# Performance work log

Hardware: AMD Instinct MI355X
Metric: run time of the kernel (lower is better)

The kernel has to match this reference:

```python
import jax, jax.numpy as jnp
import numpy as np

B, F, D_IN, D_K, D_V = 4, 4096, 1024, 128, 128


def setup_inputs() -> dict:
    key = jax.random.key(0)
    ks = jax.random.split(key, 7)
    s_in = 1.0 / np.sqrt(D_IN)
    x = jax.random.normal(ks[0], (B, F, D_IN), dtype=jnp.float32)
    # nn.Linear weights stored as (out, in); we keep (in, out) for x @ W
    Wq = jax.random.uniform(ks[1], (D_IN, D_K), jnp.float32, -s_in, s_in)
    bq = jax.random.uniform(ks[2], (D_K,), jnp.float32, -s_in, s_in)
    Wk = jax.random.uniform(ks[3], (D_IN, D_K), jnp.float32, -s_in, s_in)
    bk = jax.random.uniform(ks[4], (D_K,), jnp.float32, -s_in, s_in)
    Wv = jax.random.uniform(ks[5], (D_IN, D_V), jnp.float32, -s_in, s_in)
    bv = jax.random.uniform(ks[6], (D_V,), jnp.float32, -s_in, s_in)
    return {"x": x, "Wq": Wq, "bq": bq, "Wk": Wk, "bk": bk, "Wv": Wv, "bv": bv}


def reference(x, Wq, bq, Wk, bk, Wv, bv):
    Q = x @ Wq + bq  # (B, F, d_k)
    K = x @ Wk + bk  # (B, F, d_k)
    V = x @ Wv + bv  # (B, F, d_v)
    scale = 1.0 / jnp.sqrt(jnp.asarray(Q.shape[-1], Q.dtype))
    scores = jnp.einsum('bqd,bkd->bqk', Q, K) * scale  # (B, F, F)
    attn = jax.nn.softmax(scores, axis=-1)
    return jnp.einsum('bqk,bkd->bqd', attn, V)  # (B, F, d_v)
```

## Files before the change

### kernel.cpp

```cpp
#include <hip/hip_runtime.h>

#define TB 4
#define TF 4096
#define DIN 1024
#define DK 128
#define M_TOT (TB * TF)

typedef __attribute__((ext_vector_type(8))) short sh8;
typedef __attribute__((ext_vector_type(4))) float f32x4;

#if __has_builtin(__builtin_amdgcn_exp2f)
#define EXP2(x) __builtin_amdgcn_exp2f(x)
#else
#define EXP2(x) exp2f(x)
#endif

__device__ __forceinline__ unsigned short f2bf(float f) {
  unsigned int u = __builtin_bit_cast(unsigned int, f);
  u += 0x7FFFu + ((u >> 16) & 1u);
  return (unsigned short)(u >> 16);
}

__device__ __forceinline__ unsigned int pack_bf2(float a, float b) {
  return (unsigned int)f2bf(a) | ((unsigned int)f2bf(b) << 16);
}

__device__ __forceinline__ float bf2f(unsigned short u) {
  unsigned int x = ((unsigned int)u) << 16;
  return __builtin_bit_cast(float, x);
}

__global__ __launch_bounds__(256) void prep_wt_kernel(
    const float* __restrict__ Wq, const float* __restrict__ Wk,
    const float* __restrict__ Wv, unsigned short* __restrict__ Wf) {
  int idx = blockIdx.x * 256 + threadIdx.x;
  int j = idx & 7;
  int lane = (idx >> 3) & 63;
  int ks = (idx >> 9) & 31;
  int t = (idx >> 14) & 7;
  int p = idx >> 17;
  int col = t * 16 + (lane & 15);
  int k = ks * 32 + (lane >> 4) * 8 + j;
  const float* W = (p == 0) ? Wq : (p == 1) ? Wk : Wv;
  Wf[idx] = f2bf(W[k * DK + col]);
}

__global__ __launch_bounds__(512, 2) void proj_kernel(
    const float* __restrict__ x,
    const unsigned short* __restrict__ Wf,
    const float* __restrict__ bq, const float* __restrict__ bk,
    const float* __restrict__ bv,
    unsigned short* __restrict__ Qb,
    unsigned short* __restrict__ Kb,
    unsigned short* __restrict__ VT)
{
  const int tid = threadIdx.x;
  const int wave = tid >> 6;
  const int lane = tid & 63;
  const int lr = lane & 15;
  const int lg = lane >> 4;
  const int m0 = blockIdx.x * 64;
  const int col = wave * 16 + lr;

  __shared__ unsigned short Xlds[2][64 * 68];

  f32x4 acc[3][4];
  const f32x4 z4 = {0.f, 0.f, 0.f, 0.f};
#pragma unroll
  for (int p = 0; p < 3; ++p)
#pragma unroll
    for (int m = 0; m < 4; ++m) acc[p][m] = z4;

  const int xr = tid >> 3;
  const int xk8 = (tid & 7) * 8;
  const float* xrow = x + (size_t)(m0 + xr) * DIN + xk8;

  {
    const float4 f0 = *(const float4*)(xrow);
    const float4 f1 = *(const float4*)(xrow + 4);
    union { sh8 v; unsigned short u[8]; } U;
    U.u[0] = f2bf(f0.x); U.u[1] = f2bf(f0.y);
    U.u[2] = f2bf(f0.z); U.u[3] = f2bf(f0.w);
    U.u[4] = f2bf(f1.x); U.u[5] = f2bf(f1.y);
    U.u[6] = f2bf(f1.z); U.u[7] = f2bf(f1.w);
    *(sh8*)&Xlds[0][xr * 68 + xk8] = U.v;
  }
  __syncthreads();

  for (int t = 0; t < DIN / 64; ++t) {
    const int k0 = t * 64;
    const int cur = t & 1;

    if (t + 1 < DIN / 64) {
      const float4 f0 = *(const float4*)(xrow + k0 + 64);
      const float4 f1 = *(const float4*)(xrow + k0 + 68);
      union { sh8 v; unsigned short u[8]; } U;
      U.u[0] = f2bf(f0.x); U.u[1] = f2bf(f0.y);
      U.u[2] = f2bf(f0.z); U.u[3] = f2bf(f0.w);
      U.u[4] = f2bf(f1.x); U.u[5] = f2bf(f1.y);
      U.u[6] = f2bf(f1.z); U.u[7] = f2bf(f1.w);
      *(sh8*)&Xlds[cur ^ 1][xr * 68 + xk8] = U.v;
    }

    sh8 a[4][2];
#pragma unroll
    for (int m = 0; m < 4; ++m)
#pragma unroll
      for (int s = 0; s < 2; ++s)
        a[m][s] =
            *(const sh8*)&Xlds[cur][(m * 16 + lr) * 68 + s * 32 + lg * 8];
#pragma unroll
    for (int p = 0; p < 3; ++p) {
#pragma unroll
      for (int s = 0; s < 2; ++s) {
        sh8 b = *(const sh8*)(Wf +
                              ((size_t)((p * 8 + wave) * 32 + (k0 >> 5) + s)) *
                                  512 +
                              lane * 8);
#pragma unroll
        for (int m = 0; m < 4; ++m)
          acc[p][m] = __builtin_amdgcn_mfma_f32_16x16x32_bf16(a[m][s], b,
                                                              acc[p][m], 0, 0,
                                                              0);
      }
    }
    __syncthreads();
  }

  const float scale = 0.12751744f;
  const int b_idx = m0 >> 12;
  const float add_q = bq[col];
  const float add_k = bk[col];
  const float add_v = bv[col];
#pragma unroll
  for (int m = 0; m < 4; ++m) {
    const int rowbase = m0 + m * 16 + lg * 4;
#pragma unroll
    for (int r = 0; r < 4; ++r) {
      Qb[(size_t)(rowbase + r) * DK + col] =
          f2bf((acc[0][m][r] + add_q) * scale);
      Kb[(size_t)(rowbase + r) * DK + col] = f2bf(acc[1][m][r] + add_k);
    }
    const int fbase = (m0 & (TF - 1)) + m * 16 + lg * 4;
    ushort4 pv;
    pv.x = f2bf(acc[2][m][0] + add_v);
    pv.y = f2bf(acc[2][m][1] + add_v);
    pv.z = f2bf(acc[2][m][2] + add_v);
    pv.w = f2bf(acc[2][m][3] + add_v);
    *(ushort4*)(VT + ((size_t)b_idx * DK + col) * TF + fbase) = pv;
  }
}

template <int SPLIT>
__global__ __launch_bounds__(512, 2) void attn_part_kernel(
    const unsigned short* __restrict__ Qb, const unsigned short* __restrict__ Kb,
    const unsigned short* __restrict__ VT, unsigned short* __restrict__ Opart,
    float* __restrict__ Mpart, float* __restrict__ Lpart,
    float* __restrict__ out) {
  constexpr int CHUNK = TF / SPLIT;
  constexpr int NT = CHUNK / 64;
  const int tid = threadIdx.x;
  const int lane = tid & 63;
  const int lr = lane & 15;
  const int lg = lane >> 4;

  const int bid = blockIdx.x;
  const int xcd = bid & 7;
  const int batch = xcd >> 1;
  const int idb = ((bid >> 3) << 1) | (xcd & 1);
  const int slot = idb / SPLIT;
  const int chunk = idb % SPLIT;
  const int wave = tid >> 6;
  const int q0 = batch * TF + slot * 128 + wave * 16;
  const int kbase = chunk * CHUNK;

  __shared__ unsigned short Klds[2][64 * 136];
  __shared__ unsigned short Vlds[2][128 * 72];

  const unsigned short* Qp = Qb + (size_t)q0 * DK;
  const unsigned short* Kp = Kb + (size_t)batch * TF * DK;
  const unsigned short* Vp = VT + (size_t)batch * DK * TF;

  const int krow0 = tid >> 4, kc8 = tid & 15;
  const int vrow0 = tid >> 3, vc8 = tid & 7;

  sh8 aq[4];
#pragma unroll
  for (int dd = 0; dd < 4; ++dd)
    aq[dd] = *(const sh8*)(Qp + lr * DK + dd * 32 + lg * 8);

  const f32x4 z4 = {0.f, 0.f, 0.f, 0.f};
  f32x4 ot[8];
#pragma unroll
  for (int nb = 0; nb < 8; ++nb) ot[nb] = z4;
  float mrow = -1e30f, lrow = 0.f;

  const int srcA = lr + ((lane >> 4) & 1) * 32;
  const int srcB = srcA + 16;
  const bool chi = (lg >= 2);

#pragma unroll
  for (int i = 0; i < 2; ++i) {
    *(uint4*)&Klds[0][(krow0 + i * 32) * 136 + kc8 * 8] =
        *(const uint4*)(Kp + (size_t)(kbase + krow0 + i * 32) * DK + kc8 * 8);
    *(uint4*)&Vlds[0][(vrow0 + i * 64) * 72 + vc8 * 8] =
        *(const uint4*)(Vp + (size_t)(vrow0 + i * 64) * TF + kbase + vc8 * 8);
  }
  __syncthreads();

  for (int t = 0; t < NT; ++t) {
    const int kk0 = kbase + t * 64;
    const int cur = t & 1;

    if (t + 1 < NT) {
#pragma unroll
      for (int i = 0; i < 2; ++i) {
        *(uint4*)&Klds[cur ^ 1][(krow0 + i * 32) * 136 + kc8 * 8] =
            *(const uint4*)(Kp + (size_t)(kk0 + 64 + krow0 + i * 32) * DK +
                            kc8 * 8);
        *(uint4*)&Vlds[cur ^ 1][(vrow0 + i * 64) * 72 + vc8 * 8] =
            *(const uint4*)(Vp + (size_t)(vrow0 + i * 64) * TF + kk0 + 64 +
                            vc8 * 8);
      }
    }

    f32x4 st[4];
#pragma unroll
    for (int c = 0; c < 4; ++c) st[c] = z4;
    __builtin_amdgcn_s_setprio(1);
#pragma unroll
    for (int dd = 0; dd < 4; ++dd) {
#pragma unroll
      for (int c = 0; c < 4; ++c) {
        sh8 kb =
            *(const sh8*)&Klds[cur][(c * 16 + lr) * 136 + dd * 32 + lg * 8];
        st[c] =
            __builtin_amdgcn_mfma_f32_16x16x32_bf16(kb, aq[dd], st[c], 0, 0, 0);
      }
    }
    __builtin_amdgcn_s_setprio(0);

    float mx;
    {
      float m0a = fmaxf(fmaxf(st[0][0], st[0][1]), st[0][2]);
      float m0b = fmaxf(fmaxf(st[0][3], st[1][0]), st[1][1]);
      float m0c = fmaxf(fmaxf(st[1][2], st[1][3]), st[2][0]);
      float m0d = fmaxf(fmaxf(st[2][1], st[2][2]), st[2][3]);
      float m0e = fmaxf(fmaxf(st[3][0], st[3][1]), st[3][2]);
      float m1a = fmaxf(fmaxf(m0a, m0b), m0c);
      float m1b = fmaxf(fmaxf(m0d, m0e), st[3][3]);
      mx = fmaxf(m1a, m1b);
    }
    mx = fmaxf(mx, __shfl_xor(mx, 16));
    mx = fmaxf(mx, __shfl_xor(mx, 32));

    if (!__all(mx - mrow <= 11.5f)) {
      const float mnew = fmaxf(mrow, mx);
      const float al = EXP2(mrow - mnew);
      lrow *= al;
#pragma unroll
      for (int nb = 0; nb < 8; ++nb)
#pragma unroll
        for (int r = 0; r < 4; ++r) ot[nb][r] *= al;
      mrow = mnew;
    }

    float p[4][4];
    float rs = 0.f;
#pragma unroll
    for (int c = 0; c < 4; ++c)
#pragma unroll
      for (int r = 0; r < 4; ++r) {
        p[c][r] = EXP2(st[c][r] - mrow);
        rs += p[c][r];
      }
    rs += __shfl_xor(rs, 16);
    rs += __shfl_xor(rs, 32);
    lrow += rs;

    unsigned int up[4][2];
#pragma unroll
    for (int c = 0; c < 4; ++c) {
      up[c][0] = pack_bf2(p[c][0], p[c][1]);
      up[c][1] = pack_bf2(p[c][2], p[c][3]);
    }

#pragma unroll
    for (int ks = 0; ks < 2; ++ks) {
      unsigned int e0 = __shfl((int)up[2 * ks][0], srcA);
      unsigned int o0 = __shfl((int)up[2 * ks + 1][0], srcA);
      unsigned int e1 = __shfl((int)up[2 * ks][1], srcA);
      unsigned int o1 = __shfl((int)up[2 * ks + 1][1], srcA);
      unsigned int e2 = __shfl((int)up[2 * ks][0], srcB);
      unsigned int o2 = __shfl((int)up[2 * ks + 1][0], srcB);
      unsigned int e3 = __shfl((int)up[2 * ks][1], srcB);
      unsigned int o3 = __shfl((int)up[2 * ks + 1][1], srcB);
      union { unsigned int u[4]; sh8 v; } PA;
      PA.u[0] = chi ? o0 : e0;
      PA.u[1] = chi ? o1 : e1;
      PA.u[2] = chi ? o2 : e2;
      PA.u[3] = chi ? o3 : e3;
      __builtin_amdgcn_s_setprio(1);
#pragma unroll
      for (int nb = 0; nb < 8; ++nb) {
        sh8 vb =
            *(const sh8*)&Vlds[cur][(nb * 16 + lr) * 72 + ks * 32 + lg * 8];
        ot[nb] =
            __builtin_amdgcn_mfma_f32_16x16x32_bf16(vb, PA.v, ot[nb], 0, 0, 0);
      }
      __builtin_amdgcn_s_setprio(0);
    }

    __syncthreads();
  }

  if constexpr (SPLIT == 1) {
    const float inv = 1.0f / lrow;
#pragma unroll
    for (int nb = 0; nb < 8; ++nb) {
      float4 res = {ot[nb][0] * inv, ot[nb][1] * inv, ot[nb][2] * inv,
                    ot[nb][3] * inv};
      *(float4*)(out + (size_t)(q0 + lr) * DK + nb * 16 + lg * 4) = res;
    }
  } else {
    const int row = q0 + lr;
    if (lg == 0) {
      Mpart[(size_t)chunk * M_TOT + row] = mrow;
      Lpart[(size_t)chunk * M_TOT + row] = lrow;
    }
#pragma unroll
    for (int nb = 0; nb < 8; ++nb) {
      ushort4 res;
      res.x = f2bf(ot[nb][0]); res.y = f2bf(ot[nb][1]);
      res.z = f2bf(ot[nb][2]); res.w = f2bf(ot[nb][3]);
      *(ushort4*)(Opart + ((size_t)chunk * M_TOT + row) * DK + nb * 16 +
                  lg * 4) = res;
    }
  }
}

__global__ __launch_bounds__(256) void combine_kernel(
    const unsigned short* __restrict__ Opart, const float* __restrict__ Mpart,
    const float* __restrict__ Lpart, float* __restrict__ out, int split) {
  const int idx = blockIdx.x * 256 + threadIdx.x;
  const int row = idx >> 5;
  const int cq = (idx & 31) << 2;
  float m = -1e30f;
  for (int s = 0; s < split; ++s) m = fmaxf(m, Mpart[(size_t)s * M_TOT + row]);
  float den = 0.f;
  float4 acc = {0.f, 0.f, 0.f, 0.f};
  for (int s = 0; s < split; ++s) {
    const float w = EXP2(Mpart[(size_t)s * M_TOT + row] - m);
    den += w * Lpart[(size_t)s * M_TOT + row];
    const ushort4 v =
        *(const ushort4*)(Opart + ((size_t)s * M_TOT + row) * DK + cq);
    acc.x += w * bf2f(v.x); acc.y += w * bf2f(v.y);
    acc.z += w * bf2f(v.z); acc.w += w * bf2f(v.w);
  }
  const float inv = 1.0f / den;
  float4 res = {acc.x * inv, acc.y * inv, acc.z * inv, acc.w * inv};
  *(float4*)(out + (size_t)row * DK + cq) = res;
}

extern "C" void kernel_launch(void* const* d_in, const int* in_sizes, int n_in,
                              void* d_out, int out_size, void* d_ws,
                              size_t ws_size, hipStream_t stream) {
  const float* x = (const float*)d_in[0];
  const float* Wq = (const float*)d_in[1];
  const float* bq = (const float*)d_in[2];
  const float* Wk = (const float*)d_in[3];
  const float* bk = (const float*)d_in[4];
  const float* Wv = (const float*)d_in[5];
  const float* bv = (const float*)d_in[6];
  float* out = (float*)d_out;

  unsigned short* Wf = (unsigned short*)d_ws;
  unsigned short* Qb = Wf + 3 * DK * DIN;
  unsigned short* Kb = Qb + (size_t)M_TOT * DK;
  unsigned short* VT = Kb + (size_t)M_TOT * DK;
  unsigned short* Opart = VT + (size_t)M_TOT * DK;
  const size_t base_bytes = 2ull * (3 * DK * DIN + 3ull * M_TOT * DK);
  const size_t per_split = (size_t)M_TOT * DK * 2 + 2ull * M_TOT * 4;

  prep_wt_kernel<<<(3 * DK * DIN) / 256, 256, 0, stream>>>(Wq, Wk, Wv, Wf);
  proj_kernel<<<M_TOT / 64, 512, 0, stream>>>(x, Wf, bq, bk, bv, Qb, Kb, VT);

  int split;
  if (ws_size >= base_bytes + 4 * per_split) split = 4;
  else if (ws_size >= base_bytes + 2 * per_split) split = 2;
  else split = 1;

  float* Mpart = (float*)(Opart + (size_t)split * M_TOT * DK);
  float* Lpart = Mpart + (size_t)split * M_TOT;

  if (split == 4) {
    attn_part_kernel<4><<<128 * 4, 512, 0, stream>>>(Qb, Kb, VT, Opart, Mpart,
                                                     Lpart, out);
    combine_kernel<<<M_TOT * 32 / 256, 256, 0, stream>>>(Opart, Mpart, Lpart,
                                                         out, 4);
  } else if (split == 2) {
    attn_part_kernel<2><<<128 * 2, 512, 0, stream>>>(Qb, Kb, VT, Opart, Mpart,
                                                     Lpart, out);
    combine_kernel<<<M_TOT * 32 / 256, 256, 0, stream>>>(Opart, Mpart, Lpart,
                                                         out, 2);
  } else {
    attn_part_kernel<1><<<128, 512, 0, stream>>>(Qb, Kb, VT, nullptr, nullptr,
                                                 nullptr, out);
  }
}
```

Measured before the change: 97.30 us.

## Single-buffer K/V tiles and route P through LDS instead of shuffles

Replaces the double-buffered K/V LDS prefetch with a single buffer that is loaded synchronously each iteration between two barriers. The shuffle-based transpose of the softmax probabilities is replaced by writing them to a per-wave LDS scratch and reading them back as MFMA operands. It also drops the min-blocks-per-CU launch bound. This reduces LDS footprint and shuffle work, but gives up overlap of global loads with compute and adds an extra barrier per tile.

```diff
diff --git a/kernel.cpp b/kernel.cpp
--- a/kernel.cpp
+++ b/kernel.cpp
@@ -19,10 +19,6 @@
   unsigned int u = __builtin_bit_cast(unsigned int, f);
   u += 0x7FFFu + ((u >> 16) & 1u);
   return (unsigned short)(u >> 16);
-}
-
-__device__ __forceinline__ unsigned int pack_bf2(float a, float b) {
-  return (unsigned int)f2bf(a) | ((unsigned int)f2bf(b) << 16);
 }
 
 __device__ __forceinline__ float bf2f(unsigned short u) {
@@ -152,13 +148,12 @@
 }
 
 template <int SPLIT>
-__global__ __launch_bounds__(512, 2) void attn_part_kernel(
+__global__ __launch_bounds__(512) void attn_part_kernel(
     const unsigned short* __restrict__ Qb, const unsigned short* __restrict__ Kb,
     const unsigned short* __restrict__ VT, unsigned short* __restrict__ Opart,
     float* __restrict__ Mpart, float* __restrict__ Lpart,
     float* __restrict__ out) {
   constexpr int CHUNK = TF / SPLIT;
-  constexpr int NT = CHUNK / 64;
   const int tid = threadIdx.x;
   const int lane = tid & 63;
   const int lr = lane & 15;
@@ -174,16 +169,15 @@
   const int q0 = batch * TF + slot * 128 + wave * 16;
   const int kbase = chunk * CHUNK;
 
-  __shared__ unsigned short Klds[2][64 * 136];
-  __shared__ unsigned short Vlds[2][128 * 72];
+  __shared__ unsigned short Klds[64 * 136];
+  __shared__ unsigned short Vlds[128 * 72];
+  __shared__ unsigned short Plds[8][16 * 72];
+  unsigned short* Pw = &Plds[wave][0];
 
   const unsigned short* Qp = Qb + (size_t)q0 * DK;
   const unsigned short* Kp = Kb + (size_t)batch * TF * DK;
   const unsigned short* Vp = VT + (size_t)batch * DK * TF;
 
-  const int krow0 = tid >> 4, kc8 = tid & 15;
-  const int vrow0 = tid >> 3, vc8 = tid & 7;
-
   sh8 aq[4];
 #pragma unroll
   for (int dd = 0; dd < 4; ++dd)
@@ -195,34 +189,23 @@
   for (int nb = 0; nb < 8; ++nb) ot[nb] = z4;
   float mrow = -1e30f, lrow = 0.f;
 
-  const int srcA = lr + ((lane >> 4) & 1) * 32;
-  const int srcB = srcA + 16;
-  const bool chi = (lg >= 2);
-
-#pragma unroll
-  for (int i = 0; i < 2; ++i) {
-    *(uint4*)&Klds[0][(krow0 + i * 32) * 136 + kc8 * 8] =
-        *(const uint4*)(Kp + (size_t)(kbase + krow0 + i * 32) * DK + kc8 * 8);
-    *(uint4*)&Vlds[0][(vrow0 + i * 64) * 72 + vc8 * 8] =
-        *(const uint4*)(Vp + (size_t)(vrow0 + i * 64) * TF + kbase + vc8 * 8);
-  }
-  __syncthreads();
-
-  for (int t = 0; t < NT; ++t) {
-    const int kk0 = kbase + t * 64;
-    const int cur = t & 1;
-
-    if (t + 1 < NT) {
-#pragma unroll
-      for (int i = 0; i < 2; ++i) {
-        *(uint4*)&Klds[cur ^ 1][(krow0 + i * 32) * 136 + kc8 * 8] =
-            *(const uint4*)(Kp + (size_t)(kk0 + 64 + krow0 + i * 32) * DK +
-                            kc8 * 8);
-        *(uint4*)&Vlds[cur ^ 1][(vrow0 + i * 64) * 72 + vc8 * 8] =
-            *(const uint4*)(Vp + (size_t)(vrow0 + i * 64) * TF + kk0 + 64 +
-                            vc8 * 8);
-      }
-    }
+  for (int kk0 = kbase; kk0 < kbase + CHUNK; kk0 += 64) {
+    __syncthreads();
+#pragma unroll
+    for (int i = 0; i < 2; ++i) {
+      int c = tid + i * 512;
+      int row = c >> 4, c8 = c & 15;
+      *(uint4*)&Klds[row * 136 + c8 * 8] =
+          *(const uint4*)(Kp + (size_t)(kk0 + row) * DK + c8 * 8);
+    }
+#pragma unroll
+    for (int i = 0; i < 2; ++i) {
+      int c = tid + i * 512;
+      int row = c >> 3, c8 = c & 7;
+      *(uint4*)&Vlds[row * 72 + c8 * 8] =
+          *(const uint4*)(Vp + (size_t)row * TF + kk0 + c8 * 8);
+    }
+    __syncthreads();
 
     f32x4 st[4];
 #pragma unroll
@@ -232,8 +215,7 @@
     for (int dd = 0; dd < 4; ++dd) {
 #pragma unroll
       for (int c = 0; c < 4; ++c) {
-        sh8 kb =
-            *(const sh8*)&Klds[cur][(c * 16 + lr) * 136 + dd * 32 + lg * 8];
+        sh8 kb = *(const sh8*)&Klds[(c * 16 + lr) * 136 + dd * 32 + lg * 8];
         st[c] =
             __builtin_amdgcn_mfma_f32_16x16x32_bf16(kb, aq[dd], st[c], 0, 0, 0);
       }
@@ -265,53 +247,34 @@
       mrow = mnew;
     }
 
-    float p[4][4];
     float rs = 0.f;
 #pragma unroll
-    for (int c = 0; c < 4; ++c)
-#pragma unroll
-      for (int r = 0; r < 4; ++r) {
-        p[c][r] = EXP2(st[c][r] - mrow);
-        rs += p[c][r];
-      }
+    for (int c = 0; c < 4; ++c) {
+      float p0 = EXP2(st[c][0] - mrow);
+      float p1 = EXP2(st[c][1] - mrow);
+      float p2 = EXP2(st[c][2] - mrow);
+      float p3 = EXP2(st[c][3] - mrow);
+      rs += p0 + p1 + p2 + p3;
+      ushort4 w;
+      w.x = f2bf(p0); w.y = f2bf(p1); w.z = f2bf(p2); w.w = f2bf(p3);
+      *(ushort4*)&Pw[lr * 72 + c * 16 + lg * 4] = w;
+    }
     rs += __shfl_xor(rs, 16);
     rs += __shfl_xor(rs, 32);
     lrow += rs;
 
-    unsigned int up[4][2];
-#pragma unroll
-    for (int c = 0; c < 4; ++c) {
-      up[c][0] = pack_bf2(p[c][0], p[c][1]);
-      up[c][1] = pack_bf2(p[c][2], p[c][3]);
-    }
-
 #pragma unroll
     for (int ks = 0; ks < 2; ++ks) {
-      unsigned int e0 = __shfl((int)up[2 * ks][0], srcA);
-      unsigned int o0 = __shfl((int)up[2 * ks + 1][0], srcA);
-      unsigned int e1 = __shfl((int)up[2 * ks][1], srcA);
-      unsigned int o1 = __shfl((int)up[2 * ks + 1][1], srcA);
-      unsigned int e2 = __shfl((int)up[2 * ks][0], srcB);
-      unsigned int o2 = __shfl((int)up[2 * ks + 1][0], srcB);
-      unsigned int e3 = __shfl((int)up[2 * ks][1], srcB);
-      unsigned int o3 = __shfl((int)up[2 * ks + 1][1], srcB);
-      union { unsigned int u[4]; sh8 v; } PA;
-      PA.u[0] = chi ? o0 : e0;
-      PA.u[1] = chi ? o1 : e1;
-      PA.u[2] = chi ? o2 : e2;
-      PA.u[3] = chi ? o3 : e3;
+      sh8 pa = *(const sh8*)&Pw[lr * 72 + ks * 32 + lg * 8];
       __builtin_amdgcn_s_setprio(1);
 #pragma unroll
       for (int nb = 0; nb < 8; ++nb) {
-        sh8 vb =
-            *(const sh8*)&Vlds[cur][(nb * 16 + lr) * 72 + ks * 32 + lg * 8];
+        sh8 vb = *(const sh8*)&Vlds[(nb * 16 + lr) * 72 + ks * 32 + lg * 8];
         ot[nb] =
-            __builtin_amdgcn_mfma_f32_16x16x32_bf16(vb, PA.v, ot[nb], 0, 0, 0);
+            __builtin_amdgcn_mfma_f32_16x16x32_bf16(vb, pa, ot[nb], 0, 0, 0);
       }
       __builtin_amdgcn_s_setprio(0);
     }
-
-    __syncthreads();
   }
 
   if constexpr (SPLIT == 1) {
```

After: 91.88 us (median of 3 runs). 5.6% less time.
